# Kernel optimization log

Measured on AMD Instinct MI355X. Metric: run time of the kernel, lower is better.

## Reference

```python
import jax, jax.numpy as jnp
import numpy as np

B, N, DF, DC = 16, 4096, 128, 3
N_GROUP, K_GROUP = 1024, 16
D_IN, D_OUT = DC + DF, 256  # d_features = [131, 256]
BN_EPS = 1e-5


def farthest_point_sample(coord, n_sample):
    # coord: [B, N, 3] -> idx: [B, n_sample] (deterministic start at point 0)
    b, n, _ = coord.shape
    dist0 = jnp.full((b, n), jnp.inf, coord.dtype)
    idx0 = jnp.zeros((b,), jnp.int32)

    def step(carry, _):
        dist, last = carry
        last_pt = jnp.take_along_axis(coord, last[:, None, None].astype(jnp.int32), axis=1)  # [B,1,3]
        d = jnp.sum((coord - last_pt) ** 2, axis=-1)  # [B,N]
        dist = jnp.minimum(dist, d)
        nxt = jnp.argmax(dist, axis=1).astype(jnp.int32)
        return (dist, nxt), last

    _, idxs = jax.lax.scan(step, (dist0, idx0), None, length=n_sample)
    return jnp.swapaxes(idxs, 0, 1)  # [B, n_sample]


def knn_points(coord, center_coord, k):
    # squared distances [B, G, N]; k nearest source points per center
    d2 = jnp.sum((center_coord[:, :, None, :] - coord[:, None, :, :]) ** 2, axis=-1)
    _, idx = jax.lax.top_k(-d2, k)  # [B, G, k]
    return idx.astype(jnp.int32)


def index_points(points, idx):
    # points: [B, N, C]; idx: [B, ...] -> [B, ..., C]
    b = points.shape[0]
    batch_idx = jnp.arange(b).reshape((b,) + (1,) * (idx.ndim - 1))
    return points[batch_idx, idx]


def setup_inputs() -> dict:
    key = jax.random.key(0)
    k1, k2, k3, k4 = jax.random.split(key, 4)
    feature = jax.random.normal(k1, (B, N, DF), dtype=jnp.float32)
    coord = jax.random.normal(k2, (B, N, DC), dtype=jnp.float32)
    W = jax.random.normal(k3, (D_OUT, D_IN), dtype=jnp.float32) * (1.0 / np.sqrt(D_IN))
    b = jax.random.normal(k4, (D_OUT,), dtype=jnp.float32) * 0.01
    gamma = jnp.ones((D_OUT,), dtype=jnp.float32)
    beta = jnp.zeros((D_OUT,), dtype=jnp.float32)
    return {"feature": feature, "coord": coord, "W": W, "b": b, "gamma": gamma, "beta": beta}


def reference(feature, coord, W, b, gamma, beta):
    # --- group ---
    center_idx = farthest_point_sample(coord, N_GROUP)            # [B,G]
    center_coord = index_points(coord, center_idx)                 # [B,G,3]
    neigh_idx = knn_points(coord, center_coord, K_GROUP)           # [B,G,K]
    neigh_coord = index_points(coord, neigh_idx) - center_coord[:, :, None]  # [B,G,K,3]
    neigh_feature = jnp.concatenate([neigh_coord, index_points(feature, neigh_idx)], axis=-1)  # [B,G,K,131]
    # --- 1x1 conv + BatchNorm (train-mode batch stats, biased var) + ReLU ---
    y = jnp.einsum('bgkc,oc->bgko', neigh_feature, W) + b          # [B,G,K,256]
    mean = jnp.mean(y, axis=(0, 1, 2))
    var = jnp.mean((y - mean) ** 2, axis=(0, 1, 2))
    y = (y - mean) * jax.lax.rsqrt(var + BN_EPS) * gamma + beta
    y = jax.nn.relu(y)
    # --- max over neighbors ---
    center_feature = jnp.max(y, axis=2)                            # [B,G,256]
    return center_feature, center_coord
```

## Files before the change

### kernel.cpp

```cpp
#include <hip/hip_runtime.h>
#include <stdint.h>

#define BATCH 16
#define NPTS 4096
#define DFEAT 128
#define NGRP 1024
#define KNNK 16
#define DOUT_CH 256
#define KPAD 160
#define APAD 168
#define NGROUPS (BATCH*NGRP)
#define MROWS (NGROUPS*KNNK)
#define NWORKERS 240
#define NCHUNKS (NGROUPS/8)
#define CHUNKS_PER_BATCH (NGRP/8)
#define OUT_FEAT_ELEMS (NGROUPS*DOUT_CH)
#define KNN_SLOTS 512
#define PROG_STRIDE 16

typedef __attribute__((ext_vector_type(8))) short s16x8;
typedef __attribute__((ext_vector_type(8))) __bf16 bf16x8;
typedef __attribute__((ext_vector_type(4))) float f32x4;

union V8U { s16x8 s; bf16x8 b; };

__device__ inline unsigned short f2bf(float f) {
  unsigned u = __float_as_uint(f);
  unsigned r = 0x7FFFu + ((u >> 16) & 1u);
  return (unsigned short)((u + r) >> 16);
}

__device__ inline float sqdist3(float ax, float ay, float az,
                                float bx, float by, float bz) {
  float dx = __fsub_rn(ax, bx);
  float dy = __fsub_rn(ay, by);
  float dz = __fsub_rn(az, bz);
  return __fadd_rn(__fadd_rn(__fmul_rn(dx, dx), __fmul_rn(dy, dy)), __fmul_rn(dz, dz));
}

__device__ inline unsigned long long u64max(unsigned long long a, unsigned long long b) {
  return a > b ? a : b;
}

template<int CTRL>
__device__ inline unsigned long long dpp_max_step(unsigned long long k) {
  unsigned hi = (unsigned)(k >> 32), lo = (unsigned)k;
  unsigned hi2 = (unsigned)__builtin_amdgcn_update_dpp(0, (int)hi, CTRL, 0xF, 0xF, true);
  unsigned lo2 = (unsigned)__builtin_amdgcn_update_dpp(0, (int)lo, CTRL, 0xF, 0xF, true);
  unsigned long long k2 = ((unsigned long long)hi2 << 32) | lo2;
  return k2 > k ? k2 : k;
}
__device__ inline unsigned long long wave_max_u64(unsigned long long k) {
  k = dpp_max_step<0xB1>(k);
  k = dpp_max_step<0x4E>(k);
  k = dpp_max_step<0x141>(k);
  k = dpp_max_step<0x140>(k);
  k = dpp_max_step<0x142>(k);
  k = dpp_max_step<0x143>(k);
  return k;
}

template<int CTRL>
__device__ inline unsigned long long dpp_min_step(unsigned long long k) {
  unsigned hi = (unsigned)(k >> 32), lo = (unsigned)k;
  unsigned hi2 = (unsigned)__builtin_amdgcn_update_dpp((int)hi, (int)hi, CTRL, 0xF, 0xF, false);
  unsigned lo2 = (unsigned)__builtin_amdgcn_update_dpp((int)lo, (int)lo, CTRL, 0xF, 0xF, false);
  unsigned long long k2 = ((unsigned long long)hi2 << 32) | lo2;
  return k2 < k ? k2 : k;
}
__device__ inline unsigned long long wave_min_u64(unsigned long long k) {
  k = dpp_min_step<0xB1>(k);
  k = dpp_min_step<0x4E>(k);
  k = dpp_min_step<0x141>(k);
  k = dpp_min_step<0x140>(k);
  k = dpp_min_step<0x142>(k);
  k = dpp_min_step<0x143>(k);
  return k;
}

struct FpsSh {
  float4 c4[NPTS];
  float ocb[NGRP * 3];
  unsigned long long slots[2][4];
};
struct WrkSh {
  float wd[4][NPTS];
  float svd[4][KNN_SLOTS];
  int   svi[4][KNN_SLOTS];
  unsigned short Abuf[2][16][APAD];
  int   nidx_s[8][KNNK];
  float cent_s[8][3];
};
union ShU { FpsSh f; WrkSh w; };

__global__ __launch_bounds__(256)
void fused_kernel(const float* __restrict__ feat, const float* __restrict__ coord,
                  const float* __restrict__ W, float* __restrict__ out_coord,
                  unsigned short* __restrict__ Wb,
                  float* __restrict__ psum, float* __restrict__ psumsq,
                  float* __restrict__ wmax, float* __restrict__ wmin,
                  int* __restrict__ progress, int* __restrict__ wb_ready)
{
  __shared__ ShU sh;
  const int tid = threadIdx.x;
  const int w = tid >> 6;
  const int lane = tid & 63;

  if (blockIdx.x < BATCH) {
    const int b = blockIdx.x;
    float4* c4 = sh.f.c4;
    float* ocb = sh.f.ocb;

    const float* g = coord + (size_t)b * NPTS * 3;
    for (int p = tid; p < NPTS; p += 256)
      c4[p] = make_float4(g[3 * p], g[3 * p + 1], g[3 * p + 2], 0.f);
    __syncthreads();

    float px[16], py[16], pz[16], dist[16];
    unsigned lokey[16];
    #pragma unroll
    for (int j = 0; j < 16; ++j) {
      int p = tid + 256 * j;
      float4 c = c4[p];
      px[j] = c.x; py[j] = c.y; pz[j] = c.z;
      dist[j] = __builtin_inff();
      lokey[j] = 0xFFFFFFFFu - (unsigned)p;
    }

    float lx = c4[0].x, ly = c4[0].y, lz = c4[0].z;
    if (tid == 0) { ocb[0] = lx; ocb[1] = ly; ocb[2] = lz; }

    float* oc = out_coord + (size_t)b * NGRP * 3;
    int pend = 0;

    for (int i = 1; i < NGRP; ++i) {
      const int par = i & 1;
      unsigned long long cand[16];
      #pragma unroll
      for (int j = 0; j < 16; ++j) {
        float d  = sqdist3(px[j], py[j], pz[j], lx, ly, lz);
        float nd = fminf(dist[j], d);
        dist[j] = nd;
        cand[j] = ((unsigned long long)__float_as_uint(nd) << 32) | lokey[j];
      }
      #pragma unroll
      for (int st = 8; st >= 1; st >>= 1)
        #pragma unroll
        for (int j = 0; j < st; ++j)
          cand[j] = u64max(cand[j], cand[j + st]);
      unsigned long long best = wave_max_u64(cand[0]);
      if (lane == 63) sh.f.slots[par][w] = best;
      __syncthreads();

      if (pend) {
        if (tid == 0) {
          __threadfence();
          __hip_atomic_store(&progress[b * PROG_STRIDE], pend, __ATOMIC_RELEASE, __HIP_MEMORY_SCOPE_AGENT);
        }
        pend = 0;
      }
      if ((i & 7) == 0) {
        if (tid < 24) oc[(i - 8) * 3 + tid] = ocb[(i - 8) * 3 + tid];
        pend = i;
      }

      unsigned long long s0 = u64max(sh.f.slots[par][0], sh.f.slots[par][1]);
      unsigned long long s1 = u64max(sh.f.slots[par][2], sh.f.slots[par][3]);
      unsigned long long f = u64max(s0, s1);
      int mi = (int)(0xFFFFFFFFu - (unsigned)(f & 0xFFFFFFFFull));

      float4 cw = c4[mi];
      lx = cw.x; ly = cw.y; lz = cw.z;
      if (tid < 3) ocb[3 * i + tid] = (tid == 0) ? cw.x : ((tid == 1) ? cw.y : cw.z);
    }

    __syncthreads();
    #pragma unroll
    for (int qq = 0; qq < 12; ++qq) oc[tid + 256 * qq] = ocb[tid + 256 * qq];
    __syncthreads();
    if (tid == 0) {
      __threadfence();
      __hip_atomic_store(&progress[b * PROG_STRIDE], NGRP, __ATOMIC_RELEASE, __HIP_MEMORY_SCOPE_AGENT);
    }
    return;
  }

  const int wi = blockIdx.x - BATCH;

  if (wi == 0) {
    for (int i = tid; i < DOUT_CH * KPAD; i += 256) {
      int n = i / KPAD;
      int k = i - n * KPAD;
      float v = 0.f;
      if (k < 128)      v = W[n * 131 + 3 + k];
      else if (k < 131) v = W[n * 131 + (k - 128)];
      Wb[i] = f2bf(v);
    }
    __syncthreads();
    if (tid == 0) {
      __threadfence();
      __hip_atomic_store(wb_ready, 1, __ATOMIC_RELEASE, __HIP_MEMORY_SCOPE_AGENT);
    }
  }
  if (tid == 0) {
    while (__hip_atomic_load(wb_ready, __ATOMIC_RELAXED, __HIP_MEMORY_SCOPE_AGENT) == 0)
      __builtin_amdgcn_s_sleep(1);
    __threadfence();
  }
  __syncthreads();

  const int lr = lane & 15, q = lane >> 4;

  V8U bfrag[4][5];
  #pragma unroll
  for (int nt = 0; nt < 4; ++nt)
    #pragma unroll
    for (int kt = 0; kt < 5; ++kt) {
      int n = w * 64 + nt * 16 + lr;
      bfrag[nt][kt].s = *(const s16x8*)(Wb + n * KPAD + kt * 32 + q * 8);
    }

  for (int i = tid; i < 2 * 16 * 32; i += 256) {
    int buf = i >> 9, rr = (i >> 5) & 15, cc = 128 + (i & 31);
    sh.w.Abuf[buf][rr][cc] = 0;
  }
  float sum1[4] = {0, 0, 0, 0}, sum2[4] = {0, 0, 0, 0};
  __syncthreads();

  for (int ord = wi; ord < NCHUNKS; ord += NWORKERS) {
    const int b  = ord & 15;
    const int lc = ord >> 4;
    const int need = lc * 8 + 8;

    if (tid == 0) {
      while (__hip_atomic_load(&progress[b * PROG_STRIDE], __ATOMIC_RELAXED, __HIP_MEMORY_SCOPE_AGENT) < need)
        __builtin_amdgcn_s_sleep(16);
      __threadfence();
    }
    __syncthreads();

    if (tid < 24) sh.w.cent_s[tid / 3][tid % 3] =
        out_coord[(size_t)b * NGRP * 3 + lc * 24 + tid];
    __syncthreads();

    const float* pc = coord + (size_t)b * NPTS * 3;
    for (int k2 = 0; k2 < 2; ++k2) {
      const int k8 = w * 2 + k2;
      const float cx = sh.w.cent_s[k8][0], cy = sh.w.cent_s[k8][1], cz = sh.w.cent_s[k8][2];
      float* wd  = sh.w.wd[w];
      float* wsd = sh.w.svd[w];
      int*   wsi = sh.w.svi[w];

      float m = __builtin_inff();
      for (int tt = 0; tt < 64; ++tt) {
        int p = tt * 64 + lane;
        float d = sqdist3(cx, cy, cz, pc[3 * p], pc[3 * p + 1], pc[3 * p + 2]);
        wd[p] = d;
        m = fminf(m, d);
      }
      unsigned mb = __float_as_uint(m);
      unsigned prefix = 0u;
      for (int bit = 30; bit >= 0; --bit) {
        unsigned trial = prefix | (1u << bit);
        if (__popcll(__ballot(mb < trial)) < 16) prefix = trial;
      }
      const unsigned T = prefix;

      int base = 0;
      unsigned long long ltmask = (1ull << lane) - 1ull;
      for (int tt = 0; tt < 64; ++tt) {
        int p = tt * 64 + lane;
        float d = wd[p];
        bool keep = (__float_as_uint(d) <= T);
        unsigned long long mk = __ballot(keep);
        if (keep) {
          int pos = base + __popcll(mk & ltmask);
          if (pos < KNN_SLOTS) { wsd[pos] = d; wsi[pos] = p; }
        }
        base += __popcll(mk);
      }
      int S = base < KNN_SLOTS ? base : KNN_SLOTS;

      float rsd[8];
      #pragma unroll
      for (int k = 0; k < 8; ++k) {
        int s = lane + 64 * k;
        rsd[k] = (s < S) ? wsd[s] : __builtin_inff();
      }
      for (int r = 0; r < KNNK; ++r) {
        unsigned long long key = 0xFFFFFFFFFFFFFFFFull;
        #pragma unroll
        for (int k = 0; k < 8; ++k) {
          unsigned long long kk = ((unsigned long long)__float_as_uint(rsd[k]) << 32)
                                | (unsigned)(lane + 64 * k);
          key = kk < key ? kk : key;
        }
        key = wave_min_u64(key);
        int bs = __builtin_amdgcn_readlane((int)(unsigned)(key & 0xFFFFFFFFull), 63);
        #pragma unroll
        for (int k = 0; k < 8; ++k)
          if (lane == (bs & 63) && k == (bs >> 6)) rsd[k] = __builtin_inff();
        if (lane == 0) sh.w.nidx_s[k8][r] = wsi[bs];
      }
    }
    __syncthreads();

    auto stage = [&](int gi, int buf) {
      int r = tid >> 4, c16 = tid & 15;
      int np = sh.w.nidx_s[gi][r];
      const float* fr = feat + ((size_t)(b * NPTS + np)) * DFEAT + c16 * 8;
      float4 f0 = ((const float4*)fr)[0];
      float4 f1 = ((const float4*)fr)[1];
      s16x8 v;
      v[0] = f2bf(f0.x); v[1] = f2bf(f0.y); v[2] = f2bf(f0.z); v[3] = f2bf(f0.w);
      v[4] = f2bf(f1.x); v[5] = f2bf(f1.y); v[6] = f2bf(f1.z); v[7] = f2bf(f1.w);
      *(s16x8*)&sh.w.Abuf[buf][r][c16 * 8] = v;
      if (tid < 16) {
        int np2 = sh.w.nidx_s[gi][tid];
        const float* p = coord + ((size_t)(b * NPTS + np2)) * 3;
        sh.w.Abuf[buf][tid][128] = f2bf(p[0] - sh.w.cent_s[gi][0]);
        sh.w.Abuf[buf][tid][129] = f2bf(p[1] - sh.w.cent_s[gi][1]);
        sh.w.Abuf[buf][tid][130] = f2bf(p[2] - sh.w.cent_s[gi][2]);
      }
    };

    stage(0, 0);
    __syncthreads();

    for (int gi = 0; gi < 8; ++gi) {
      int cur = gi & 1;
      if (gi < 7) stage(gi + 1, cur ^ 1);

      f32x4 acc[4];
      #pragma unroll
      for (int nt = 0; nt < 4; ++nt) acc[nt] = (f32x4)0.0f;
      #pragma unroll
      for (int kt = 0; kt < 5; ++kt) {
        V8U a;
        a.s = *(const s16x8*)&sh.w.Abuf[cur][lr][kt * 32 + q * 8];
        #pragma unroll
        for (int nt = 0; nt < 4; ++nt)
          acc[nt] = __builtin_amdgcn_mfma_f32_16x16x32_bf16(a.b, bfrag[nt][kt].b, acc[nt], 0, 0, 0);
      }
      int gidx = (b * CHUNKS_PER_BATCH + lc) * 8 + gi;
      #pragma unroll
      for (int nt = 0; nt < 4; ++nt) {
        float r0 = acc[nt][0], r1 = acc[nt][1], r2 = acc[nt][2], r3 = acc[nt][3];
        float mx = fmaxf(fmaxf(r0, r1), fmaxf(r2, r3));
        float mn = fminf(fminf(r0, r1), fminf(r2, r3));
        sum1[nt] += r0 + r1 + r2 + r3;
        sum2[nt] += r0 * r0 + r1 * r1 + r2 * r2 + r3 * r3;
        mx = fmaxf(mx, __shfl_xor(mx, 16)); mn = fminf(mn, __shfl_xor(mn, 16));
        mx = fmaxf(mx, __shfl_xor(mx, 32)); mn = fminf(mn, __shfl_xor(mn, 32));
        if (q == 0) {
          int col = w * 64 + nt * 16 + lr;
          wmax[(size_t)gidx * DOUT_CH + col] = mx;
          wmin[(size_t)gidx * DOUT_CH + col] = mn;
        }
      }
      __syncthreads();
    }
  }

  #pragma unroll
  for (int nt = 0; nt < 4; ++nt) {
    float s1 = sum1[nt], s2 = sum2[nt];
    s1 += __shfl_xor(s1, 16); s2 += __shfl_xor(s2, 16);
    s1 += __shfl_xor(s1, 32); s2 += __shfl_xor(s2, 32);
    if (q == 0) {
      int col = w * 64 + nt * 16 + lr;
      psum[(size_t)col * NWORKERS + wi]   = s1;
      psumsq[(size_t)col * NWORKERS + wi] = s2;
    }
  }
}

__global__ __launch_bounds__(256)
void stats_kernel(const float* __restrict__ psum, const float* __restrict__ psumsq,
                  const float* __restrict__ gamma, const float* __restrict__ beta,
                  float* __restrict__ sc, float* __restrict__ tc)
{
  const int c = blockIdx.x;
  const int tid = threadIdx.x, lane = tid & 63, w = tid >> 6;
  float s1 = 0.f, s2 = 0.f;
  for (int r = tid; r < NWORKERS; r += 256) {
    s1 += psum[(size_t)c * NWORKERS + r];
    s2 += psumsq[(size_t)c * NWORKERS + r];
  }
  #pragma unroll
  for (int off = 1; off < 64; off <<= 1) { s1 += __shfl_xor(s1, off); s2 += __shfl_xor(s2, off); }
  __shared__ float a1[4], a2[4];
  if (lane == 0) { a1[w] = s1; a2[w] = s2; }
  __syncthreads();
  if (tid == 0) {
    float S1 = a1[0] + a1[1] + a1[2] + a1[3];
    float S2 = a2[0] + a2[1] + a2[2] + a2[3];
    const float inv = 1.0f / (float)MROWS;
    float mean = S1 * inv;
    float var  = S2 * inv - mean * mean;
    float rs = rsqrtf(var + 1e-5f);
    float s = gamma[c] * rs;
    sc[c] = s;
    tc[c] = beta[c] - mean * s;
  }
}

__global__ __launch_bounds__(256)
void final_kernel(const float* __restrict__ wmax, const float* __restrict__ wmin,
                  const float* __restrict__ sc, const float* __restrict__ tc,
                  float* __restrict__ out)
{
  int i4 = blockIdx.x * 256 + threadIdx.x;
  int base = i4 * 4;
  int c = base & (DOUT_CH - 1);
  float4 mx = *(const float4*)(wmax + base);
  float4 mn = *(const float4*)(wmin + base);
  float4 sv = *(const float4*)(sc + c);
  float4 tv = *(const float4*)(tc + c);
  float4 o;
  o.x = fmaxf(fmaf(sv.x, (sv.x > 0.f ? mx.x : mn.x), tv.x), 0.f);
  o.y = fmaxf(fmaf(sv.y, (sv.y > 0.f ? mx.y : mn.y), tv.y), 0.f);
  o.z = fmaxf(fmaf(sv.z, (sv.z > 0.f ? mx.z : mn.z), tv.z), 0.f);
  o.w = fmaxf(fmaf(sv.w, (sv.w > 0.f ? mx.w : mn.w), tv.w), 0.f);
  *(float4*)(out + base) = o;
}

extern "C" void kernel_launch(void* const* d_in, const int* in_sizes, int n_in,
                              void* d_out, int out_size, void* d_ws, size_t ws_size,
                              hipStream_t stream)
{
  const float* feature = (const float*)d_in[0];
  const float* coord   = (const float*)d_in[1];
  const float* W       = (const float*)d_in[2];
  const float* gamma   = (const float*)d_in[4];
  const float* beta    = (const float*)d_in[5];
  float* out = (float*)d_out;
  float* out_coord = out + OUT_FEAT_ELEMS;

  char* ws = (char*)d_ws;
  int*            flags  = (int*)(ws + 0);
  unsigned short* Wb     = (unsigned short*)(ws + 4096);
  float*          psum   = (float*)(ws + (1 << 20));
  float*          psumsq = (float*)(ws + (2 << 20));
  float*          sc     = (float*)(ws + (3 << 20));
  float*          tc     = (float*)(ws + (3 << 20) + 4096);
  float*          wmax   = (float*)(ws + (8 << 20));
  float*          wmin   = (float*)(ws + (8 << 20) + (size_t)OUT_FEAT_ELEMS * 4);
  int* progress = flags;
  int* wb_ready = flags + BATCH * PROG_STRIDE;

  hipMemsetAsync(flags, 0, (BATCH * PROG_STRIDE + 16) * sizeof(int), stream);

  hipLaunchKernelGGL(fused_kernel, dim3(BATCH + NWORKERS), dim3(256), 0, stream,
                     feature, coord, W, out_coord, Wb,
                     psum, psumsq, wmax, wmin, progress, wb_ready);
  hipLaunchKernelGGL(stats_kernel, dim3(DOUT_CH), dim3(256), 0, stream,
                     psum, psumsq, gamma, beta, sc, tc);
  hipLaunchKernelGGL(final_kernel, dim3(OUT_FEAT_ELEMS / 1024), dim3(256), 0, stream,
                     wmax, wmin, sc, tc, out);
}
```

Measured before the change: 799.4 us.

## Morton-sort FPS points per thread and skip distance updates via bounding-box bound

Before farthest point sampling, points are bucketed on an 8x8x8 Morton grid with a shared-memory histogram and prefix sum, so each thread owns 16 spatially close points and keeps their bounding box. Each FPS iteration computes a lower bound on the distance from the newly selected point to the thread's box. When that bound is at least the thread's current max min-distance, the distance update is skipped and the cached best key is reused. This cuts the per-iteration FPS arithmetic on the serial critical path, at the cost of a sort prologue, more shared memory and divergent per-lane work. The wave reduction and block sync still run every iteration.

```diff
diff --git a/kernel.cpp b/kernel.cpp
--- a/kernel.cpp
+++ b/kernel.cpp
@@ -78,10 +78,18 @@
   return k;
 }
 
+__device__ inline int expand3(int v) {
+  return (v & 1) | ((v & 2) << 2) | ((v & 4) << 4);
+}
+
 struct FpsSh {
   float4 c4[NPTS];
   float ocb[NGRP * 3];
   unsigned long long slots[2][4];
+  int hist[512];
+  unsigned short order[NPTS];
+  int wsum[4];
+  float mm[4][6];
 };
 struct WrkSh {
   float wd[4][NPTS];
@@ -111,20 +119,93 @@
     float4* c4 = sh.f.c4;
     float* ocb = sh.f.ocb;
 
-    const float* g = coord + (size_t)b * NPTS * 3;
-    for (int p = tid; p < NPTS; p += 256)
-      c4[p] = make_float4(g[3 * p], g[3 * p + 1], g[3 * p + 2], 0.f);
-    __syncthreads();
-
-    float px[16], py[16], pz[16], dist[16];
-    unsigned lokey[16];
+    float mnx = __builtin_inff(), mny = __builtin_inff(), mnz = __builtin_inff();
+    float mxx = -__builtin_inff(), mxy = -__builtin_inff(), mxz = -__builtin_inff();
+    {
+      const float* g = coord + (size_t)b * NPTS * 3;
+      for (int p = tid; p < NPTS; p += 256) {
+        float x = g[3 * p], y = g[3 * p + 1], z = g[3 * p + 2];
+        c4[p] = make_float4(x, y, z, 0.f);
+        mnx = fminf(mnx, x); mxx = fmaxf(mxx, x);
+        mny = fminf(mny, y); mxy = fmaxf(mxy, y);
+        mnz = fminf(mnz, z); mxz = fmaxf(mxz, z);
+      }
+    }
+    #pragma unroll
+    for (int off = 32; off >= 1; off >>= 1) {
+      mnx = fminf(mnx, __shfl_xor(mnx, off)); mxx = fmaxf(mxx, __shfl_xor(mxx, off));
+      mny = fminf(mny, __shfl_xor(mny, off)); mxy = fmaxf(mxy, __shfl_xor(mxy, off));
+      mnz = fminf(mnz, __shfl_xor(mnz, off)); mxz = fmaxf(mxz, __shfl_xor(mxz, off));
+    }
+    if (lane == 0) {
+      sh.f.mm[w][0] = mnx; sh.f.mm[w][1] = mny; sh.f.mm[w][2] = mnz;
+      sh.f.mm[w][3] = mxx; sh.f.mm[w][4] = mxy; sh.f.mm[w][5] = mxz;
+    }
+    for (int k = tid; k < 512; k += 256) sh.f.hist[k] = 0;
+    __syncthreads();
+    mnx = fminf(fminf(sh.f.mm[0][0], sh.f.mm[1][0]), fminf(sh.f.mm[2][0], sh.f.mm[3][0]));
+    mny = fminf(fminf(sh.f.mm[0][1], sh.f.mm[1][1]), fminf(sh.f.mm[2][1], sh.f.mm[3][1]));
+    mnz = fminf(fminf(sh.f.mm[0][2], sh.f.mm[1][2]), fminf(sh.f.mm[2][2], sh.f.mm[3][2]));
+    mxx = fmaxf(fmaxf(sh.f.mm[0][3], sh.f.mm[1][3]), fmaxf(sh.f.mm[2][3], sh.f.mm[3][3]));
+    mxy = fmaxf(fmaxf(sh.f.mm[0][4], sh.f.mm[1][4]), fmaxf(sh.f.mm[2][4], sh.f.mm[3][4]));
+    mxz = fmaxf(fmaxf(sh.f.mm[0][5], sh.f.mm[1][5]), fmaxf(sh.f.mm[2][5], sh.f.mm[3][5]));
+    const float sx = 7.9999f / fmaxf(mxx - mnx, 1e-20f);
+    const float sy = 7.9999f / fmaxf(mxy - mny, 1e-20f);
+    const float sz = 7.9999f / fmaxf(mxz - mnz, 1e-20f);
+
+    int mcode[16];
     #pragma unroll
     for (int j = 0; j < 16; ++j) {
       int p = tid + 256 * j;
       float4 c = c4[p];
+      int qx = (int)((c.x - mnx) * sx); qx = qx < 0 ? 0 : (qx > 7 ? 7 : qx);
+      int qy = (int)((c.y - mny) * sy); qy = qy < 0 ? 0 : (qy > 7 ? 7 : qy);
+      int qz = (int)((c.z - mnz) * sz); qz = qz < 0 ? 0 : (qz > 7 ? 7 : qz);
+      mcode[j] = (expand3(qx) << 2) | (expand3(qy) << 1) | expand3(qz);
+      atomicAdd(&sh.f.hist[mcode[j]], 1);
+    }
+    __syncthreads();
+    {
+      int a0 = sh.f.hist[2 * tid], a1 = sh.f.hist[2 * tid + 1];
+      int s = a0 + a1;
+      int inc = s;
+      #pragma unroll
+      for (int off = 1; off < 64; off <<= 1) {
+        int n = __shfl_up(inc, off);
+        if (lane >= off) inc += n;
+      }
+      if (lane == 63) sh.f.wsum[w] = inc;
+      __syncthreads();
+      int woff = 0;
+      #pragma unroll
+      for (int k = 0; k < 4; ++k) if (k < w) woff += sh.f.wsum[k];
+      int ex = woff + inc - s;
+      sh.f.hist[2 * tid] = ex;
+      sh.f.hist[2 * tid + 1] = ex + a0;
+    }
+    __syncthreads();
+    #pragma unroll
+    for (int j = 0; j < 16; ++j) {
+      int p = tid + 256 * j;
+      int pos = atomicAdd(&sh.f.hist[mcode[j]], 1);
+      sh.f.order[pos] = (unsigned short)p;
+    }
+    __syncthreads();
+
+    float px[16], py[16], pz[16], dist[16];
+    unsigned lokey[16];
+    float bxl = __builtin_inff(), byl = __builtin_inff(), bzl = __builtin_inff();
+    float bxh = -__builtin_inff(), byh = -__builtin_inff(), bzh = -__builtin_inff();
+    #pragma unroll
+    for (int j = 0; j < 16; ++j) {
+      int op = sh.f.order[tid * 16 + j];
+      float4 c = c4[op];
       px[j] = c.x; py[j] = c.y; pz[j] = c.z;
       dist[j] = __builtin_inff();
-      lokey[j] = 0xFFFFFFFFu - (unsigned)p;
+      lokey[j] = 0xFFFFFFFFu - (unsigned)op;
+      bxl = fminf(bxl, c.x); bxh = fmaxf(bxh, c.x);
+      byl = fminf(byl, c.y); byh = fmaxf(byh, c.y);
+      bzl = fminf(bzl, c.z); bzh = fmaxf(bzh, c.z);
     }
 
     float lx = c4[0].x, ly = c4[0].y, lz = c4[0].z;
@@ -132,23 +213,39 @@
 
     float* oc = out_coord + (size_t)b * NGRP * 3;
     int pend = 0;
+    unsigned long long ckey = (unsigned long long)0x7F800000u << 32;
 
     for (int i = 1; i < NGRP; ++i) {
       const int par = i & 1;
-      unsigned long long cand[16];
-      #pragma unroll
-      for (int j = 0; j < 16; ++j) {
-        float d  = sqdist3(px[j], py[j], pz[j], lx, ly, lz);
-        float nd = fminf(dist[j], d);
-        dist[j] = nd;
-        cand[j] = ((unsigned long long)__float_as_uint(nd) << 32) | lokey[j];
-      }
-      #pragma unroll
-      for (int st = 8; st >= 1; st >>= 1)
+
+      float ex = fmaxf(fmaxf(bxl - lx, lx - bxh), 0.f);
+      float ey = fmaxf(fmaxf(byl - ly, ly - byh), 0.f);
+      float ez = fmaxf(fmaxf(bzl - lz, lz - bzh), 0.f);
+      float lb = (ex * ex + ey * ey + ez * ez) * 0.99999f;
+      float lmaxd = __uint_as_float((unsigned)(ckey >> 32));
+
+      unsigned long long best;
+      if (lb < lmaxd) {
+        unsigned long long cand[16];
         #pragma unroll
-        for (int j = 0; j < st; ++j)
-          cand[j] = u64max(cand[j], cand[j + st]);
-      unsigned long long best = wave_max_u64(cand[0]);
+        for (int j = 0; j < 16; ++j) {
+          float d  = sqdist3(px[j], py[j], pz[j], lx, ly, lz);
+          float nd = fminf(dist[j], d);
+          dist[j] = nd;
+          cand[j] = ((unsigned long long)__float_as_uint(nd) << 32) | lokey[j];
+        }
+        #pragma unroll
+        for (int st = 8; st >= 1; st >>= 1)
+          #pragma unroll
+          for (int j = 0; j < st; ++j)
+            cand[j] = u64max(cand[j], cand[j + st]);
+        best = cand[0];
+        ckey = best;
+      } else {
+        best = ckey;
+      }
+
+      best = wave_max_u64(best);
       if (lane == 63) sh.f.slots[par][w] = best;
       __syncthreads();
 
```

Result: slower. 834.0 us (+4.3%).

## Fold BN stats and final epilogue into fused kernel via last-block grid sync

Applied to the files above, without the earlier changes.

Removes the separate stats and final kernels. Each worker block increments a done counter, the last block reduces the per-worker partial sums into scale and shift and raises a ready flag, and every worker then applies the BN, ReLU and max epilogue to its own chunks. This saves two kernel launches and their gaps, at the cost of one block doing the reduction serially while the others spin on the flag. It also drops the explicit thread fences before release stores, publishes FPS progress every 32 groups instead of 8, and transposes the partial-sum layout.

```diff
diff --git a/kernel.cpp b/kernel.cpp
--- a/kernel.cpp
+++ b/kernel.cpp
@@ -90,16 +90,21 @@
   unsigned short Abuf[2][16][APAD];
   int   nidx_s[8][KNNK];
   float cent_s[8][3];
+  int   statflag;
 };
 union ShU { FpsSh f; WrkSh w; };
 
 __global__ __launch_bounds__(256)
 void fused_kernel(const float* __restrict__ feat, const float* __restrict__ coord,
-                  const float* __restrict__ W, float* __restrict__ out_coord,
+                  const float* __restrict__ W, const float* __restrict__ gamma,
+                  const float* __restrict__ beta, float* __restrict__ out,
+                  float* __restrict__ out_coord,
                   unsigned short* __restrict__ Wb,
                   float* __restrict__ psum, float* __restrict__ psumsq,
+                  float* __restrict__ scg, float* __restrict__ tcg,
                   float* __restrict__ wmax, float* __restrict__ wmin,
-                  int* __restrict__ progress, int* __restrict__ wb_ready)
+                  int* __restrict__ progress, int* __restrict__ wb_ready,
+                  int* __restrict__ done, int* __restrict__ sc_ready)
 {
   __shared__ ShU sh;
   const int tid = threadIdx.x;
@@ -153,14 +158,12 @@
       __syncthreads();
 
       if (pend) {
-        if (tid == 0) {
-          __threadfence();
+        if (tid == 0)
           __hip_atomic_store(&progress[b * PROG_STRIDE], pend, __ATOMIC_RELEASE, __HIP_MEMORY_SCOPE_AGENT);
-        }
         pend = 0;
       }
-      if ((i & 7) == 0) {
-        if (tid < 24) oc[(i - 8) * 3 + tid] = ocb[(i - 8) * 3 + tid];
+      if ((i & 31) == 0) {
+        if (tid < 96) oc[(i - 32) * 3 + tid] = ocb[(i - 32) * 3 + tid];
         pend = i;
       }
 
@@ -178,10 +181,8 @@
     #pragma unroll
     for (int qq = 0; qq < 12; ++qq) oc[tid + 256 * qq] = ocb[tid + 256 * qq];
     __syncthreads();
-    if (tid == 0) {
-      __threadfence();
+    if (tid == 0)
       __hip_atomic_store(&progress[b * PROG_STRIDE], NGRP, __ATOMIC_RELEASE, __HIP_MEMORY_SCOPE_AGENT);
-    }
     return;
   }
 
@@ -197,10 +198,8 @@
       Wb[i] = f2bf(v);
     }
     __syncthreads();
-    if (tid == 0) {
-      __threadfence();
+    if (tid == 0)
       __hip_atomic_store(wb_ready, 1, __ATOMIC_RELEASE, __HIP_MEMORY_SCOPE_AGENT);
-    }
   }
   if (tid == 0) {
     while (__hip_atomic_load(wb_ready, __ATOMIC_RELAXED, __HIP_MEMORY_SCOPE_AGENT) == 0)
@@ -369,60 +368,61 @@
     s1 += __shfl_xor(s1, 32); s2 += __shfl_xor(s2, 32);
     if (q == 0) {
       int col = w * 64 + nt * 16 + lr;
-      psum[(size_t)col * NWORKERS + wi]   = s1;
-      psumsq[(size_t)col * NWORKERS + wi] = s2;
-    }
-  }
-}
-
-__global__ __launch_bounds__(256)
-void stats_kernel(const float* __restrict__ psum, const float* __restrict__ psumsq,
-                  const float* __restrict__ gamma, const float* __restrict__ beta,
-                  float* __restrict__ sc, float* __restrict__ tc)
-{
-  const int c = blockIdx.x;
-  const int tid = threadIdx.x, lane = tid & 63, w = tid >> 6;
-  float s1 = 0.f, s2 = 0.f;
-  for (int r = tid; r < NWORKERS; r += 256) {
-    s1 += psum[(size_t)c * NWORKERS + r];
-    s2 += psumsq[(size_t)c * NWORKERS + r];
-  }
-  #pragma unroll
-  for (int off = 1; off < 64; off <<= 1) { s1 += __shfl_xor(s1, off); s2 += __shfl_xor(s2, off); }
-  __shared__ float a1[4], a2[4];
-  if (lane == 0) { a1[w] = s1; a2[w] = s2; }
+      psum[wi * DOUT_CH + col]   = s1;
+      psumsq[wi * DOUT_CH + col] = s2;
+    }
+  }
   __syncthreads();
   if (tid == 0) {
-    float S1 = a1[0] + a1[1] + a1[2] + a1[3];
-    float S2 = a2[0] + a2[1] + a2[2] + a2[3];
+    int old = __hip_atomic_fetch_add(done, 1, __ATOMIC_ACQ_REL, __HIP_MEMORY_SCOPE_AGENT);
+    sh.w.statflag = (old == NWORKERS - 1) ? 1 : 0;
+  }
+  __syncthreads();
+
+  if (sh.w.statflag) {
+    float s1 = 0.f, s2 = 0.f;
+    for (int r = 0; r < NWORKERS; ++r) {
+      s1 += psum[r * DOUT_CH + tid];
+      s2 += psumsq[r * DOUT_CH + tid];
+    }
     const float inv = 1.0f / (float)MROWS;
-    float mean = S1 * inv;
-    float var  = S2 * inv - mean * mean;
+    float mean = s1 * inv;
+    float var  = s2 * inv - mean * mean;
     float rs = rsqrtf(var + 1e-5f);
-    float s = gamma[c] * rs;
-    sc[c] = s;
-    tc[c] = beta[c] - mean * s;
-  }
-}
-
-__global__ __launch_bounds__(256)
-void final_kernel(const float* __restrict__ wmax, const float* __restrict__ wmin,
-                  const float* __restrict__ sc, const float* __restrict__ tc,
-                  float* __restrict__ out)
-{
-  int i4 = blockIdx.x * 256 + threadIdx.x;
-  int base = i4 * 4;
-  int c = base & (DOUT_CH - 1);
-  float4 mx = *(const float4*)(wmax + base);
-  float4 mn = *(const float4*)(wmin + base);
-  float4 sv = *(const float4*)(sc + c);
-  float4 tv = *(const float4*)(tc + c);
-  float4 o;
-  o.x = fmaxf(fmaf(sv.x, (sv.x > 0.f ? mx.x : mn.x), tv.x), 0.f);
-  o.y = fmaxf(fmaf(sv.y, (sv.y > 0.f ? mx.y : mn.y), tv.y), 0.f);
-  o.z = fmaxf(fmaf(sv.z, (sv.z > 0.f ? mx.z : mn.z), tv.z), 0.f);
-  o.w = fmaxf(fmaf(sv.w, (sv.w > 0.f ? mx.w : mn.w), tv.w), 0.f);
-  *(float4*)(out + base) = o;
+    float s = gamma[tid] * rs;
+    scg[tid] = s;
+    tcg[tid] = beta[tid] - mean * s;
+    __syncthreads();
+    if (tid == 0)
+      __hip_atomic_store(sc_ready, 1, __ATOMIC_RELEASE, __HIP_MEMORY_SCOPE_AGENT);
+  }
+
+  if (tid == 0) {
+    while (__hip_atomic_load(sc_ready, __ATOMIC_RELAXED, __HIP_MEMORY_SCOPE_AGENT) == 0)
+      __builtin_amdgcn_s_sleep(8);
+    __threadfence();
+  }
+  __syncthreads();
+
+  for (int ord = wi; ord < NCHUNKS; ord += NWORKERS) {
+    const int b  = ord & 15;
+    const int lc = ord >> 4;
+    size_t base = (size_t)((b * CHUNKS_PER_BATCH + lc) * 8) * DOUT_CH;
+    for (int t = tid; t < 512; t += 256) {
+      int off = t * 4;
+      int c = off & (DOUT_CH - 1);
+      float4 mx = *(const float4*)(wmax + base + off);
+      float4 mn = *(const float4*)(wmin + base + off);
+      float4 sv = *(const float4*)(scg + c);
+      float4 tv = *(const float4*)(tcg + c);
+      float4 o;
+      o.x = fmaxf(fmaf(sv.x, (sv.x > 0.f ? mx.x : mn.x), tv.x), 0.f);
+      o.y = fmaxf(fmaf(sv.y, (sv.y > 0.f ? mx.y : mn.y), tv.y), 0.f);
+      o.z = fmaxf(fmaf(sv.z, (sv.z > 0.f ? mx.z : mn.z), tv.z), 0.f);
+      o.w = fmaxf(fmaf(sv.w, (sv.w > 0.f ? mx.w : mn.w), tv.w), 0.f);
+      *(float4*)(out + base + off) = o;
+    }
+  }
 }
 
 extern "C" void kernel_launch(void* const* d_in, const int* in_sizes, int n_in,
@@ -442,20 +442,19 @@
   unsigned short* Wb     = (unsigned short*)(ws + 4096);
   float*          psum   = (float*)(ws + (1 << 20));
   float*          psumsq = (float*)(ws + (2 << 20));
-  float*          sc     = (float*)(ws + (3 << 20));
-  float*          tc     = (float*)(ws + (3 << 20) + 4096);
+  float*          scg    = (float*)(ws + (3 << 20));
+  float*          tcg    = (float*)(ws + (3 << 20) + 4096);
   float*          wmax   = (float*)(ws + (8 << 20));
   float*          wmin   = (float*)(ws + (8 << 20) + (size_t)OUT_FEAT_ELEMS * 4);
   int* progress = flags;
   int* wb_ready = flags + BATCH * PROG_STRIDE;
-
-  hipMemsetAsync(flags, 0, (BATCH * PROG_STRIDE + 16) * sizeof(int), stream);
+  int* done     = flags + BATCH * PROG_STRIDE + 16;
+  int* sc_ready = flags + BATCH * PROG_STRIDE + 32;
+
+  hipMemsetAsync(flags, 0, 2048, stream);
 
   hipLaunchKernelGGL(fused_kernel, dim3(BATCH + NWORKERS), dim3(256), 0, stream,
-                     feature, coord, W, out_coord, Wb,
-                     psum, psumsq, wmax, wmin, progress, wb_ready);
-  hipLaunchKernelGGL(stats_kernel, dim3(DOUT_CH), dim3(256), 0, stream,
-                     psum, psumsq, gamma, beta, sc, tc);
-  hipLaunchKernelGGL(final_kernel, dim3(OUT_FEAT_ELEMS / 1024), dim3(256), 0, stream,
-                     wmax, wmin, sc, tc, out);
-}
+                     feature, coord, W, gamma, beta, out, out_coord, Wb,
+                     psum, psumsq, scg, tcg, wmax, wmin,
+                     progress, wb_ready, done, sc_ready);
+}
```

Measured after the change: 827.4 us. 1.03x slower.
